# Optimization experiments

Hardware: AMD Instinct MI355X
Metric: run time of the kernel (lower is better)

## Reference

```python
import jax, jax.numpy as jnp
import numpy as np

NUM_HEADS = 12
TOP_K = 4
LN_EPS = 1e-5


def _ln(x, w, b):
    m = jnp.mean(x, -1, keepdims=True)
    v = jnp.mean((x - m) ** 2, -1, keepdims=True)
    return (x - m) * jax.lax.rsqrt(v + LN_EPS) * w + b


def _attn(x, qkv_w, qkv_b, proj_w, proj_b):
    B, N, C = x.shape
    hd = C // NUM_HEADS
    qkv = (x @ qkv_w + qkv_b).reshape(B, N, 3, NUM_HEADS, hd)
    q, k, v = jnp.moveaxis(qkv, 2, 0)  # each [B,N,H,hd]
    attn = jax.nn.softmax(jnp.einsum('bnhd,bmhd->bhnm', q * hd ** -0.5, k), axis=-1)
    out = jnp.einsum('bhnm,bmhd->bnhd', attn, v).reshape(B, N, C)
    return out @ proj_w + proj_b


def _moe(x2, gate_w, w1, b1, w2, b2):
    # x2: [tokens, D]; vmoe-style token top-k gating (eval mode, no noise)
    Tt = x2.shape[0]
    E = gate_w.shape[1]
    probs = jax.nn.softmax(x2 @ gate_w, axis=-1)            # [tokens, E]
    topv, topi = jax.lax.top_k(probs, TOP_K)                # [tokens, K]
    combine = jnp.zeros((Tt, E), x2.dtype).at[jnp.arange(Tt)[:, None], topi].set(topv)
    h = jax.nn.gelu(jnp.einsum('td,edh->teh', x2, w1) + b1[None], approximate=False)
    y = jnp.einsum('teh,ehd->ted', h, w2) + b2[None]
    return jnp.einsum('ted,te->td', y, combine)


def reference(x, ln1a_w, ln1a_b, qkv_wa, qkv_ba, proj_wa, proj_ba, ln2a_w, ln2a_b,
              fc1_w, fc1_b, fc2_w, fc2_b,
              ln1b_w, ln1b_b, qkv_wb, qkv_bb, proj_wb, proj_bb, ln2b_w, ln2b_b,
              gate_w, w1, b1, w2, b2, head_w, head_b,
              shared_masks, agg_mask):
    B, N, D = x.shape
    # dense ViT block
    x = x + _attn(_ln(x, ln1a_w, ln1a_b), qkv_wa, qkv_ba, proj_wa, proj_ba)
    h = _ln(x, ln2a_w, ln2a_b)
    x = x + (jax.nn.gelu(h @ fc1_w + fc1_b, approximate=False) @ fc2_w + fc2_b)
    # MoE ViT block
    x = x + _attn(_ln(x, ln1b_w, ln1b_b), qkv_wb, qkv_bb, proj_wb, proj_bb)
    h = _ln(x, ln2b_w, ln2b_b).reshape(B * N, D)
    x = x + _moe(h, gate_w, w1, b1, w2, b2).reshape(B, N, D)
    # per-task heads + masked multi-task aggregation (Aggregation.forward)
    task_out = jnp.einsum('bnd,tdo->tbno', x, head_w) + head_b[:, None, None, :]
    valid = (shared_masks & agg_mask[None]).astype(x.dtype)[..., None]  # [T,B,N,1]
    summed = (task_out * valid).sum(0)
    count = valid.sum(0)
    return summed / (count + 1e-6)


def setup_inputs() -> dict:
    key = jax.random.key(0)
    ks = jax.random.split(key, 32)
    B, N, D, HID, E, T = 8, 197, 768, 3072, 8, 8
    f = lambda k, shape: (jax.random.normal(k, shape, jnp.float32) * 0.02)
    return {
        'x': jax.random.normal(ks[0], (B, N, D), jnp.float32),
        'ln1a_w': jnp.ones((D,)), 'ln1a_b': jnp.zeros((D,)),
        'qkv_wa': f(ks[1], (D, 3 * D)), 'qkv_ba': jnp.zeros((3 * D,)),
        'proj_wa': f(ks[2], (D, D)), 'proj_ba': jnp.zeros((D,)),
        'ln2a_w': jnp.ones((D,)), 'ln2a_b': jnp.zeros((D,)),
        'fc1_w': f(ks[3], (D, HID)), 'fc1_b': jnp.zeros((HID,)),
        'fc2_w': f(ks[4], (HID, D)), 'fc2_b': jnp.zeros((D,)),
        'ln1b_w': jnp.ones((D,)), 'ln1b_b': jnp.zeros((D,)),
        'qkv_wb': f(ks[5], (D, 3 * D)), 'qkv_bb': jnp.zeros((3 * D,)),
        'proj_wb': f(ks[6], (D, D)), 'proj_bb': jnp.zeros((D,)),
        'ln2b_w': jnp.ones((D,)), 'ln2b_b': jnp.zeros((D,)),
        'gate_w': f(ks[7], (D, E)),
        'w1': f(ks[8], (E, D, HID)), 'b1': jnp.zeros((E, HID)),
        'w2': f(ks[9], (E, HID, D)), 'b2': jnp.zeros((E, D)),
        'head_w': f(ks[10], (T, D, D)), 'head_b': jnp.zeros((T, D)),
        'shared_masks': jax.random.bernoulli(ks[11], 0.5, (T, B, N)),
        'agg_mask': jax.random.bernoulli(ks[12], 0.5, (B, N)),
    }
```

## Files before the change

### kernel.cpp

```cpp
#include <hip/hip_runtime.h>
#include <hip/hip_bf16.h>

#define DEV static __device__ __forceinline__

typedef short bfx8 __attribute__((ext_vector_type(8)));
typedef float fx4  __attribute__((ext_vector_type(4)));

DEV float bf2f(__hip_bfloat16 h) { return __bfloat162float(h); }
DEV __hip_bfloat16 f2bf(float f) { return __float2bfloat16(f); }
DEV float uLO(unsigned u) { return __uint_as_float(u << 16); }
DEV float uHI(unsigned u) { return __uint_as_float(u & 0xffff0000u); }
DEV unsigned short f2bfu(float f) { __hip_bfloat16 h = __float2bfloat16(f); return *(unsigned short*)&h; }

DEV float wave_sum(float v) {
#pragma unroll
  for (int o = 32; o; o >>= 1) v += __shfl_xor(v, o, 64);
  return v;
}

#define GLD_LDS16(gp, lp) __builtin_amdgcn_global_load_lds( \
    (__attribute__((address_space(1))) void*)(gp),          \
    (__attribute__((address_space(3))) void*)(lp), 16, 0, 0)

__global__ __launch_bounds__(256) void transpose_k(
    const float* __restrict__ src, __hip_bfloat16* __restrict__ dst,
    int R, int C)
{
  __shared__ float tile[32][33];
  size_t off = (size_t)blockIdx.z * R * C;
  src += off; dst += off;
  int c0 = blockIdx.x * 32, r0 = blockIdx.y * 32;
#pragma unroll
  for (int i = 0; i < 32; i += 8)
    tile[threadIdx.y + i][threadIdx.x] =
        src[(size_t)(r0 + threadIdx.y + i) * C + c0 + threadIdx.x];
  __syncthreads();
#pragma unroll
  for (int i = 0; i < 32; i += 8)
    dst[(size_t)(c0 + threadIdx.y + i) * R + r0 + threadIdx.x] =
        f2bf(tile[threadIdx.x][threadIdx.y + i]);
}

enum { EPI_STORE = 0, EPI_GELU = 1, EPI_RESADD = 2, EPI_MOE = 3,
       EPI_GELU_R = 4, EPI_MOEP = 5, EPI_HEAD_R = 6 };

template <int MODE>
__global__ __launch_bounds__(256) void gemm_bt(
    const __hip_bfloat16* __restrict__ A,
    const __hip_bfloat16* __restrict__ BT,
    const float* __restrict__ bias,
    int M, int N, int K, int splitK, int taskBase,
    long long strideBz, long long strideBiasz, long long strideAz, long long strideCz,
    __hip_bfloat16* __restrict__ Cb, float* __restrict__ Cf,
    const float* __restrict__ combine, const int* __restrict__ rt)
{
  constexpr bool ROUTED = (MODE == EPI_GELU_R || MODE == EPI_MOEP || MODE == EPI_HEAD_R);
  constexpr bool GATHER = (MODE == EPI_GELU_R || MODE == EPI_HEAD_R);
  __shared__ __hip_bfloat16 sA[128 * 32];
  __shared__ __hip_bfloat16 sB[128 * 32];
  const int tid = threadIdx.x;
  const int wave = tid >> 6, lane = tid & 63;
  const int quad = lane >> 4, l16 = lane & 15;
  const int z = blockIdx.z;
  const int zt = z / splitK;
  const int kc = z - zt * splitK;
  const int task = taskBase + zt;
  const int Ksub = K / splitK;
  const int kbeg = kc * Ksub;
  const int m0 = blockIdx.y * 128, n0 = blockIdx.x * 128;

  int Meff = M;
  int rtb = 0;
  const int* ilist = nullptr;
  if (ROUTED) {
    const int base = (MODE == EPI_HEAD_R) ? 8 : 0;
    Meff = rt[base + zt];
    ilist = rt + 24 + (size_t)base * M + (size_t)zt * M;
    if (MODE == EPI_MOEP) rtb = rt[16 + zt];
    if (m0 >= Meff) return;
  }

  A += (size_t)zt * strideAz;
  if (MODE != EPI_MOEP) Cb += (size_t)zt * strideCz;
  const __hip_bfloat16* Bz = BT + (size_t)zt * strideBz;
  const float* biasz = bias + (size_t)zt * strideBiasz;
  const int wm = (wave >> 1) * 64, wn = (wave & 1) * 64;

  fx4 acc[4][4];
#pragma unroll
  for (int i = 0; i < 4; ++i)
#pragma unroll
    for (int j = 0; j < 4; ++j) acc[i][j] = (fx4){0.f, 0.f, 0.f, 0.f};

  const int c0 = tid, c1 = tid + 256;
  const int mlim = Meff - 1;
  int gm0 = m0 + (c0 >> 2); if (gm0 > mlim) gm0 = mlim;
  int gm1 = m0 + (c1 >> 2); if (gm1 > mlim) gm1 = mlim;
  const int ar0 = GATHER ? ilist[gm0] : gm0;
  const int ar1 = GATHER ? ilist[gm1] : gm1;
  const int ak0 = (c0 & 3) * 8, ak1 = (c1 & 3) * 8;
  const __hip_bfloat16* pa0 = A + (size_t)ar0 * K + kbeg + ak0;
  const __hip_bfloat16* pa1 = A + (size_t)ar1 * K + kbeg + ak1;
  const __hip_bfloat16* pb0 = Bz + (size_t)(n0 + (c0 >> 2)) * K + kbeg + ak0;
  const __hip_bfloat16* pb1 = Bz + (size_t)(n0 + (c1 >> 2)) * K + kbeg + ak1;

  for (int kk = 0; kk < Ksub; kk += 32) {
    GLD_LDS16(pa0 + kk, &sA[c0 * 8]);
    GLD_LDS16(pa1 + kk, &sA[c1 * 8]);
    GLD_LDS16(pb0 + kk, &sB[c0 * 8]);
    GLD_LDS16(pb1 + kk, &sB[c1 * 8]);
    __syncthreads();
    bfx8 af[4], bfr[4];
#pragma unroll
    for (int i = 0; i < 4; ++i)
      af[i] = *(const bfx8*)(&sA[(wm + i * 16 + l16) * 32 + quad * 8]);
#pragma unroll
    for (int j = 0; j < 4; ++j)
      bfr[j] = *(const bfx8*)(&sB[(wn + j * 16 + l16) * 32 + quad * 8]);
#pragma unroll
    for (int i = 0; i < 4; ++i)
#pragma unroll
      for (int j = 0; j < 4; ++j)
        acc[i][j] = __builtin_amdgcn_mfma_f32_16x16x32_bf16(af[i], bfr[j], acc[i][j], 0, 0, 0);
    __syncthreads();
  }

  const int mb = m0 + wm + quad * 4;
  const int nb = n0 + wn + l16;
#pragma unroll
  for (int i = 0; i < 4; ++i) {
#pragma unroll
    for (int rr = 0; rr < 4; ++rr) {
      const int m = mb + i * 16 + rr;
      if (m >= Meff) continue;
      int orow = m;
      if (MODE == EPI_HEAD_R) orow = ilist[m];
#pragma unroll
      for (int j = 0; j < 4; ++j) {
        const int n = nb + j * 16;
        float v = acc[i][j][rr];
        if (MODE == EPI_STORE) {
          Cb[(size_t)m * N + n] = f2bf(v + biasz[n]);
        } else if (MODE == EPI_GELU || MODE == EPI_GELU_R) {
          float t = v + biasz[n];
          Cb[(size_t)m * N + n] = f2bf(0.5f * t * (1.f + erff(t * 0.70710678118654752f)));
        } else if (MODE == EPI_RESADD) {
          if (kc == 0) v += biasz[n];
          atomicAdd(&Cf[(size_t)m * N + n], v);
        } else if (MODE == EPI_MOE) {
          float s = combine[m * 8 + task];
          if (s != 0.f) {
            if (kc == 0) v += biasz[n];
            atomicAdd(&Cf[(size_t)m * N + n], s * v);
          }
        } else if (MODE == EPI_MOEP) {
          if (kc == 0) v += biasz[n];
          Cf[(size_t)kc * strideCz + (size_t)(rtb + m) * N + n] = v;
        } else {
          atomicAdd(&Cf[(size_t)orow * N + n], v + biasz[n]);
        }
      }
    }
  }
}

__global__ __launch_bounds__(256) void attn_mfma_k(
    const __hip_bfloat16* __restrict__ qkvb, __hip_bfloat16* __restrict__ outb)
{
  __shared__ __align__(16) unsigned short VT[64 * 232];
  __shared__ __align__(16) unsigned short Pst[4][16 * 232];
  const int tid = threadIdx.x;
  const int chunk = blockIdx.x & 3;
  const int bh = blockIdx.x >> 2;
  const int b = bh / 12, h = bh - b * 12;
  const size_t tokBase = (size_t)b * 197;
  const __hip_bfloat16* qkvh = qkvb + tokBase * 2304 + (size_t)h * 64;

  for (int idx = tid; idx < 197 * 32; idx += 256) {
    int j = idx >> 5, dp = idx & 31;
    unsigned pv = *(const unsigned*)(qkvh + (size_t)j * 2304 + 1536 + dp * 2);
    VT[(2 * dp) * 232 + j]     = (unsigned short)(pv & 0xffffu);
    VT[(2 * dp + 1) * 232 + j] = (unsigned short)(pv >> 16);
  }
  for (int idx = tid; idx < 64 * 35; idx += 256) {
    int r = idx / 35, c = 197 + idx % 35;
    VT[r * 232 + c] = 0;
  }
  __syncthreads();

  const int wave = tid >> 6, lane = tid & 63;
  const int quad = lane >> 4, l16 = lane & 15;
  const int mt = chunk * 4 + wave;
  if (mt >= 13) return;

  {
    int r = lane >> 2, c = 208 + (lane & 3) * 4;
    *(uint2*)&Pst[wave][r * 232 + c] = (uint2){0u, 0u};
  }

  int tq = mt * 16 + l16; if (tq > 196) tq = 196;
  const bfx8 af0 = *(const bfx8*)(qkvh + (size_t)tq * 2304 + quad * 8);
  const bfx8 af1 = *(const bfx8*)(qkvh + (size_t)tq * 2304 + 32 + quad * 8);

  fx4 sv[13];
#pragma unroll
  for (int n0 = 0; n0 < 13; ++n0) {
    int tk = n0 * 16 + l16; if (tk > 196) tk = 196;
    const __hip_bfloat16* kp = qkvh + (size_t)tk * 2304 + 768;
    bfx8 bf0 = *(const bfx8*)(kp + quad * 8);
    bfx8 bf1 = *(const bfx8*)(kp + 32 + quad * 8);
    fx4 a = (fx4){0.f, 0.f, 0.f, 0.f};
    a = __builtin_amdgcn_mfma_f32_16x16x32_bf16(af0, bf0, a, 0, 0, 0);
    a = __builtin_amdgcn_mfma_f32_16x16x32_bf16(af1, bf1, a, 0, 0, 0);
    sv[n0] = a;
  }

  float inv[4];
#pragma unroll
  for (int rr = 0; rr < 4; ++rr) {
    float mx = -3.0e38f;
#pragma unroll
    for (int n0 = 0; n0 < 13; ++n0) {
      bool ok = (n0 < 12) | (l16 < 5);
      float s = ok ? sv[n0][rr] * 0.125f : -3.0e38f;
      sv[n0][rr] = s;
      mx = fmaxf(mx, s);
    }
#pragma unroll
    for (int o = 1; o < 16; o <<= 1) mx = fmaxf(mx, __shfl_xor(mx, o, 64));
    float sum = 0.f;
#pragma unroll
    for (int n0 = 0; n0 < 13; ++n0) {
      float s = sv[n0][rr];
      float e = (s > -1.0e38f) ? __expf(s - mx) : 0.f;
      sv[n0][rr] = e;
      sum += e;
    }
#pragma unroll
    for (int o = 1; o < 16; o <<= 1) sum += __shfl_xor(sum, o, 64);
    inv[rr] = 1.f / sum;
    const int row = quad * 4 + rr;
#pragma unroll
    for (int n0 = 0; n0 < 13; ++n0)
      Pst[wave][row * 232 + n0 * 16 + l16] = f2bfu(sv[n0][rr]);
  }

  fx4 pv[4];
#pragma unroll
  for (int nd = 0; nd < 4; ++nd) pv[nd] = (fx4){0.f, 0.f, 0.f, 0.f};
#pragma unroll
  for (int kk = 0; kk < 7; ++kk) {
    bfx8 paf = *(const bfx8*)&Pst[wave][l16 * 232 + kk * 32 + quad * 8];
#pragma unroll
    for (int nd = 0; nd < 4; ++nd) {
      bfx8 bfv = *(const bfx8*)&VT[(nd * 16 + l16) * 232 + kk * 32 + quad * 8];
      pv[nd] = __builtin_amdgcn_mfma_f32_16x16x32_bf16(paf, bfv, pv[nd], 0, 0, 0);
    }
  }

#pragma unroll
  for (int rr = 0; rr < 4; ++rr) {
    const int row = quad * 4 + rr;
#pragma unroll
    for (int n0 = 0; n0 < 13; ++n0) {
      float e = sv[n0][rr];
      Pst[wave][row * 232 + n0 * 16 + l16] = f2bfu(e - uLO(f2bfu(e)));
    }
  }

#pragma unroll
  for (int kk = 0; kk < 7; ++kk) {
    bfx8 paf = *(const bfx8*)&Pst[wave][l16 * 232 + kk * 32 + quad * 8];
#pragma unroll
    for (int nd = 0; nd < 4; ++nd) {
      bfx8 bfv = *(const bfx8*)&VT[(nd * 16 + l16) * 232 + kk * 32 + quad * 8];
      pv[nd] = __builtin_amdgcn_mfma_f32_16x16x32_bf16(paf, bfv, pv[nd], 0, 0, 0);
    }
  }

#pragma unroll
  for (int rr = 0; rr < 4; ++rr) {
    int m = mt * 16 + quad * 4 + rr;
    if (m > 196) continue;
    __hip_bfloat16* op = outb + (tokBase + m) * 768 + (size_t)h * 64;
#pragma unroll
    for (int nd = 0; nd < 4; ++nd)
      op[nd * 16 + l16] = f2bf(pv[nd][rr] * inv[rr]);
  }
}

__global__ __launch_bounds__(256) void ln_k(
    const float* __restrict__ xf, const float* __restrict__ w,
    const float* __restrict__ b, __hip_bfloat16* __restrict__ out, int T)
{
  int wv = threadIdx.x >> 6, lane = threadIdx.x & 63;
  int t = blockIdx.x * 4 + wv;
  if (t >= T) return;
  const float* row = xf + (size_t)t * 768;
  float v[12]; float s = 0.f;
#pragma unroll
  for (int i = 0; i < 12; ++i) { v[i] = row[lane + i * 64]; s += v[i]; }
  s = wave_sum(s);
  float mean = s * (1.f / 768.f);
  float q = 0.f;
#pragma unroll
  for (int i = 0; i < 12; ++i) { float d = v[i] - mean; q += d * d; }
  q = wave_sum(q);
  float rstd = rsqrtf(q * (1.f / 768.f) + 1e-5f);
#pragma unroll
  for (int i = 0; i < 12; ++i) {
    int d = lane + i * 64;
    out[(size_t)t * 768 + d] = f2bf((v[i] - mean) * rstd * w[d] + b[d]);
  }
}

__global__ __launch_bounds__(256) void gate_k(
    const float* __restrict__ xf, const float* __restrict__ lw,
    const float* __restrict__ lb, const float* __restrict__ gw,
    float* __restrict__ combine, int* __restrict__ rt, int* __restrict__ smap,
    __hip_bfloat16* __restrict__ lnbout, int T)
{
  int wv = threadIdx.x >> 6, lane = threadIdx.x & 63;
  int t = blockIdx.x * 4 + wv;
  if (t >= T) return;
  const float* row = xf + (size_t)t * 768;
  float v[12]; float s = 0.f;
#pragma unroll
  for (int i = 0; i < 12; ++i) { v[i] = row[lane + i * 64]; s += v[i]; }
  s = wave_sum(s);
  float mean = s * (1.f / 768.f);
  float qv = 0.f;
#pragma unroll
  for (int i = 0; i < 12; ++i) { float d = v[i] - mean; qv += d * d; }
  qv = wave_sum(qv);
  float rstd = rsqrtf(qv * (1.f / 768.f) + 1e-5f);
  float acc[8];
#pragma unroll
  for (int e = 0; e < 8; ++e) acc[e] = 0.f;
#pragma unroll
  for (int i = 0; i < 12; ++i) {
    int d = lane + i * 64;
    float xn = (v[i] - mean) * rstd * lw[d] + lb[d];
    lnbout[(size_t)t * 768 + d] = f2bf(xn);
    float4 g0 = *(const float4*)(gw + (size_t)d * 8);
    float4 g1 = *(const float4*)(gw + (size_t)d * 8 + 4);
    acc[0] += xn * g0.x; acc[1] += xn * g0.y;
    acc[2] += xn * g0.z; acc[3] += xn * g0.w;
    acc[4] += xn * g1.x; acc[5] += xn * g1.y;
    acc[6] += xn * g1.z; acc[7] += xn * g1.w;
  }
#pragma unroll
  for (int e = 0; e < 8; ++e) acc[e] = wave_sum(acc[e]);
  float mx = acc[0];
#pragma unroll
  for (int e = 1; e < 8; ++e) mx = fmaxf(mx, acc[e]);
  float p[8]; float se = 0.f;
#pragma unroll
  for (int e = 0; e < 8; ++e) { p[e] = __expf(acc[e] - mx); se += p[e]; }
  float inv = 1.f / se;
#pragma unroll
  for (int e = 0; e < 8; ++e) p[e] *= inv;
  float outv[8]; bool used[8];
#pragma unroll
  for (int e = 0; e < 8; ++e) { outv[e] = 0.f; used[e] = false; }
  for (int k = 0; k < 4; ++k) {
    int best = -1; float bv = -1.f;
#pragma unroll
    for (int e = 0; e < 8; ++e) if (!used[e] && p[e] > bv) { bv = p[e]; best = e; }
#pragma unroll
    for (int e = 0; e < 8; ++e) if (e == best) { used[e] = true; outv[e] = bv; }
  }
#pragma unroll
  for (int e = 0; e < 8; ++e) if (lane == e) combine[(size_t)t * 8 + e] = outv[e];
#pragma unroll
  for (int e = 0; e < 8; ++e)
    if (lane == e && outv[e] != 0.f) {
      int slot = atomicAdd(&rt[e], 1);
      rt[24 + e * T + slot] = t;
      smap[(size_t)t * 8 + e] = slot;
    }
}

__global__ void prefix_k(int* __restrict__ rt) {
  if (threadIdx.x == 0) {
    int s = 0;
#pragma unroll
    for (int e = 0; e < 8; ++e) { rt[16 + e] = s; s += rt[e]; }
  }
}

__global__ __launch_bounds__(256) void combine_k(
    const float* __restrict__ y, const float* __restrict__ combine,
    const int* __restrict__ rt, const int* __restrict__ smap,
    float* __restrict__ xf, int T, int CAP)
{
  int wv = threadIdx.x >> 6, lane = threadIdx.x & 63;
  int t = blockIdx.x * 4 + wv;
  if (t >= T) return;
  float acc[12];
#pragma unroll
  for (int i = 0; i < 12; ++i) acc[i] = 0.f;
  for (int e = 0; e < 8; ++e) {
    float s = combine[(size_t)t * 8 + e];
    if (s != 0.f) {
      int r = rt[16 + e] + smap[(size_t)t * 8 + e];
      const float* y0 = y + (size_t)r * 768;
      const float* y1 = y0 + (size_t)CAP * 768;
#pragma unroll
      for (int i = 0; i < 12; ++i)
        acc[i] += s * (y0[lane + i * 64] + y1[lane + i * 64]);
    }
  }
  float* xr = xf + (size_t)t * 768;
#pragma unroll
  for (int i = 0; i < 12; ++i) xr[lane + i * 64] += acc[i];
}

__global__ void mask_k(const int* __restrict__ sm, const int* __restrict__ am,
                       float* __restrict__ cnt, int* __restrict__ rt, int T)
{
  int t = blockIdx.x * 256 + threadIdx.x;
  if (t >= T) return;
  int a = am[t] != 0;
  float c = 0.f;
#pragma unroll
  for (int tt = 0; tt < 8; ++tt) {
    int vv = (sm[tt * T + t] != 0) & a;
    if (vv) {
      int slot = atomicAdd(&rt[8 + tt], 1);
      rt[24 + 8 * T + tt * T + slot] = t;
    }
    c += (float)vv;
  }
  cnt[t] = c;
}

__global__ void f2b_k(const float* __restrict__ in, __hip_bfloat16* __restrict__ out, int n) {
  int i = blockIdx.x * 256 + threadIdx.x;
  if (i < n) out[i] = f2bf(in[i]);
}
__global__ void final_k(float* __restrict__ out, const float* __restrict__ cnt, int n) {
  int i = blockIdx.x * 256 + threadIdx.x;
  if (i < n) out[i] = out[i] / (cnt[i / 768] + 1e-6f);
}

extern "C" void kernel_launch(void* const* d_in, const int* in_sizes, int n_in,
                              void* d_out, int out_size, void* d_ws, size_t ws_size,
                              hipStream_t stream)
{
  (void)in_sizes; (void)n_in; (void)out_size;
  const int Ttok = 8 * 197;
  const int D = 768, HID = 3072;
  const int CAP = 4 * Ttok;

  const float* x       = (const float*)d_in[0];
  const float* ln1a_w  = (const float*)d_in[1];
  const float* ln1a_b  = (const float*)d_in[2];
  const float* qkv_wa  = (const float*)d_in[3];
  const float* qkv_ba  = (const float*)d_in[4];
  const float* proj_wa = (const float*)d_in[5];
  const float* proj_ba = (const float*)d_in[6];
  const float* ln2a_w  = (const float*)d_in[7];
  const float* ln2a_b  = (const float*)d_in[8];
  const float* fc1_w   = (const float*)d_in[9];
  const float* fc1_b   = (const float*)d_in[10];
  const float* fc2_w   = (const float*)d_in[11];
  const float* fc2_b   = (const float*)d_in[12];
  const float* ln1b_w  = (const float*)d_in[13];
  const float* ln1b_b  = (const float*)d_in[14];
  const float* qkv_wb  = (const float*)d_in[15];
  const float* qkv_bb  = (const float*)d_in[16];
  const float* proj_wb = (const float*)d_in[17];
  const float* proj_bb = (const float*)d_in[18];
  const float* ln2b_w  = (const float*)d_in[19];
  const float* ln2b_b  = (const float*)d_in[20];
  const float* gate_w  = (const float*)d_in[21];
  const float* w1      = (const float*)d_in[22];
  const float* b1      = (const float*)d_in[23];
  const float* w2      = (const float*)d_in[24];
  const float* b2      = (const float*)d_in[25];
  const float* head_w  = (const float*)d_in[26];
  const float* head_b  = (const float*)d_in[27];
  const int* shared_masks = (const int*)d_in[28];
  const int* agg_mask     = (const int*)d_in[29];
  float* out           = (float*)d_out;

  char* wsp = (char*)d_ws;
  auto alloc = [&](size_t bytes) { char* p = wsp; wsp += (bytes + 255) & ~(size_t)255; return p; };
  float* xf             = (float*)alloc((size_t)Ttok * D * 4);
  __hip_bfloat16* lnb   = (__hip_bfloat16*)alloc((size_t)Ttok * D * 2);
  __hip_bfloat16* qkvb  = (__hip_bfloat16*)alloc((size_t)Ttok * 3 * D * 2);
  __hip_bfloat16* attnb = (__hip_bfloat16*)alloc((size_t)Ttok * D * 2);
  __hip_bfloat16* h1    = (__hip_bfloat16*)alloc((size_t)Ttok * HID * 2);
  float* combine        = (float*)alloc((size_t)Ttok * 8 * 4);
  float* cnt            = (float*)alloc((size_t)Ttok * 4);
  int* rt               = (int*)alloc((size_t)(24 + 16 * Ttok) * 4);
  int* smap             = (int*)alloc((size_t)Ttok * 8 * 4);
  __hip_bfloat16* qkvaT = (__hip_bfloat16*)alloc((size_t)D * 3 * D * 2);
  __hip_bfloat16* projaT= (__hip_bfloat16*)alloc((size_t)D * D * 2);
  __hip_bfloat16* fc1T  = (__hip_bfloat16*)alloc((size_t)D * HID * 2);
  __hip_bfloat16* fc2T  = (__hip_bfloat16*)alloc((size_t)D * HID * 2);
  __hip_bfloat16* qkvbT = (__hip_bfloat16*)alloc((size_t)D * 3 * D * 2);
  __hip_bfloat16* projbT= (__hip_bfloat16*)alloc((size_t)D * D * 2);
  __hip_bfloat16* headT = (__hip_bfloat16*)alloc((size_t)8 * D * D * 2);
  __hip_bfloat16* wT    = (__hip_bfloat16*)alloc((size_t)D * HID * 2);

  const size_t used = (size_t)(wsp - (char*)d_ws);
  const size_t extraNeed = 2 * ((size_t)8 * D * HID * 2 + 255)
                         + ((size_t)8 * Ttok * HID * 2 + 255)
                         + (2 * (size_t)CAP * D * 4 + 255);
  const bool batched = (ws_size >= used + extraNeed);
  __hip_bfloat16* w1T8 = nullptr; __hip_bfloat16* w2T8 = nullptr; __hip_bfloat16* h1_8 = nullptr;
  float* yb = nullptr;
  if (batched) {
    w1T8 = (__hip_bfloat16*)alloc((size_t)8 * D * HID * 2);
    w2T8 = (__hip_bfloat16*)alloc((size_t)8 * D * HID * 2);
    h1_8 = (__hip_bfloat16*)alloc((size_t)8 * Ttok * HID * 2);
    yb   = (float*)alloc(2 * (size_t)CAP * D * 4);
  }

  dim3 tb(32, 8);
  transpose_k<<<dim3(3*D/32, D/32, 1), tb, 0, stream>>>(qkv_wa, qkvaT, D, 3*D);
  transpose_k<<<dim3(D/32, D/32, 1),   tb, 0, stream>>>(proj_wa, projaT, D, D);
  transpose_k<<<dim3(HID/32, D/32, 1), tb, 0, stream>>>(fc1_w, fc1T, D, HID);
  transpose_k<<<dim3(D/32, HID/32, 1), tb, 0, stream>>>(fc2_w, fc2T, HID, D);
  transpose_k<<<dim3(3*D/32, D/32, 1), tb, 0, stream>>>(qkv_wb, qkvbT, D, 3*D);
  transpose_k<<<dim3(D/32, D/32, 1),   tb, 0, stream>>>(proj_wb, projbT, D, D);
  transpose_k<<<dim3(D/32, D/32, 8),   tb, 0, stream>>>(head_w, headT, D, D);
  if (batched) {
    transpose_k<<<dim3(HID/32, D/32, 8), tb, 0, stream>>>(w1, w1T8, D, HID);
    transpose_k<<<dim3(D/32, HID/32, 8), tb, 0, stream>>>(w2, w2T8, HID, D);
  }

  const int nTok = Ttok * D;
  hipMemcpyAsync(xf, x, (size_t)nTok * 4, hipMemcpyDeviceToDevice, stream);
  hipMemsetAsync(rt, 0, 64, stream);
  mask_k<<<(Ttok + 255)/256, 256, 0, stream>>>(shared_masks, agg_mask, cnt, rt, Ttok);
  hipMemsetAsync(out, 0, (size_t)nTok * 4, stream);

  const int lnGrid = (Ttok + 3) / 4;
  dim3 g_qkv(3*D/128, 13, 1);
  dim3 g_proj(D/128, 13, 4);
  dim3 g_fc1(HID/128, 13, 1);
  dim3 g_fc2(D/128, 13, 4);
  dim3 g_head(D/128, 13, 8);
  const int attnGrid = 96 * 4;

  ln_k<<<lnGrid, 256, 0, stream>>>(xf, ln1a_w, ln1a_b, lnb, Ttok);
  gemm_bt<EPI_STORE><<<g_qkv, 256, 0, stream>>>(lnb, qkvaT, qkv_ba, Ttok, 3*D, D, 1, 0, 0, 0, 0, 0, qkvb, nullptr, nullptr, nullptr);
  attn_mfma_k<<<attnGrid, 256, 0, stream>>>(qkvb, attnb);
  gemm_bt<EPI_RESADD><<<g_proj, 256, 0, stream>>>(attnb, projaT, proj_ba, Ttok, D, D, 4, 0, 0, 0, 0, 0, nullptr, xf, nullptr, nullptr);
  ln_k<<<lnGrid, 256, 0, stream>>>(xf, ln2a_w, ln2a_b, lnb, Ttok);
  gemm_bt<EPI_GELU><<<g_fc1, 256, 0, stream>>>(lnb, fc1T, fc1_b, Ttok, HID, D, 1, 0, 0, 0, 0, 0, h1, nullptr, nullptr, nullptr);
  gemm_bt<EPI_RESADD><<<g_fc2, 256, 0, stream>>>(h1, fc2T, fc2_b, Ttok, D, HID, 4, 0, 0, 0, 0, 0, nullptr, xf, nullptr, nullptr);

  ln_k<<<lnGrid, 256, 0, stream>>>(xf, ln1b_w, ln1b_b, lnb, Ttok);
  gemm_bt<EPI_STORE><<<g_qkv, 256, 0, stream>>>(lnb, qkvbT, qkv_bb, Ttok, 3*D, D, 1, 0, 0, 0, 0, 0, qkvb, nullptr, nullptr, nullptr);
  attn_mfma_k<<<attnGrid, 256, 0, stream>>>(qkvb, attnb);
  gemm_bt<EPI_RESADD><<<g_proj, 256, 0, stream>>>(attnb, projbT, proj_bb, Ttok, D, D, 4, 0, 0, 0, 0, 0, nullptr, xf, nullptr, nullptr);
  gate_k<<<lnGrid, 256, 0, stream>>>(xf, ln2b_w, ln2b_b, gate_w, combine, rt, smap, lnb, Ttok);
  prefix_k<<<1, 64, 0, stream>>>(rt);
  if (batched) {
    gemm_bt<EPI_GELU_R><<<dim3(HID/128, 13, 8), 256, 0, stream>>>(
        lnb, w1T8, b1, Ttok, HID, D, 1, 0,
        (long long)D*HID, HID, 0, (long long)Ttok*HID, h1_8, nullptr, nullptr, rt);
    gemm_bt<EPI_MOEP><<<dim3(D/128, 13, 16), 256, 0, stream>>>(
        h1_8, w2T8, b2, Ttok, D, HID, 2, 0,
        (long long)HID*D, D, (long long)Ttok*HID, (long long)CAP*D, nullptr, yb, nullptr, rt);
    combine_k<<<lnGrid, 256, 0, stream>>>(yb, combine, rt, smap, xf, Ttok, CAP);
  } else {
    for (int e = 0; e < 8; ++e) {
      transpose_k<<<dim3(HID/32, D/32, 1), tb, 0, stream>>>(w1 + (size_t)e*D*HID, wT, D, HID);
      gemm_bt<EPI_GELU><<<g_fc1, 256, 0, stream>>>(lnb, wT, b1 + (size_t)e*HID, Ttok, HID, D, 1, 0, 0, 0, 0, 0, h1, nullptr, nullptr, nullptr);
      transpose_k<<<dim3(D/32, HID/32, 1), tb, 0, stream>>>(w2 + (size_t)e*HID*D, wT, HID, D);
      gemm_bt<EPI_MOE><<<g_fc2, 256, 0, stream>>>(h1, wT, b2 + (size_t)e*D, Ttok, D, HID, 4, e, 0, 0, 0, 0, nullptr, xf, combine, nullptr);
    }
  }

  f2b_k<<<(nTok + 255)/256, 256, 0, stream>>>(xf, lnb, nTok);
  gemm_bt<EPI_HEAD_R><<<g_head, 256, 0, stream>>>(lnb, headT, head_b, Ttok, D, D, 1, 0, (long long)D*D, D, 0, 0, nullptr, out, nullptr, rt);
  final_k<<<(nTok + 255)/256, 256, 0, stream>>>(out, cnt, nTok);
}
```

Measured before the change: 870.2 us.

## Double-buffer GEMM LDS tiles, batch weight transposes, fuse bf16 cast into combine

The GEMM k-loop now double-buffers its A and B LDS tiles, so global-to-LDS loads for the next k-step are issued while MFMAs run on the current one, and one barrier per iteration is removed. The nine weight transpose launches are merged into one kernel driven by a descriptor table. The combine kernel also writes the bf16 copy of the residual, which removes a separate f2b pass in the batched path. The cost is doubled GEMM LDS use (32KB per block), which may lower occupancy.

Result: faster. 834.3 us (-4.1%).

```diff
diff --git a/kernel.cpp b/kernel.cpp
--- a/kernel.cpp
+++ b/kernel.cpp
@@ -9,7 +9,6 @@
 DEV float bf2f(__hip_bfloat16 h) { return __bfloat162float(h); }
 DEV __hip_bfloat16 f2bf(float f) { return __float2bfloat16(f); }
 DEV float uLO(unsigned u) { return __uint_as_float(u << 16); }
-DEV float uHI(unsigned u) { return __uint_as_float(u & 0xffff0000u); }
 DEV unsigned short f2bfu(float f) { __hip_bfloat16 h = __float2bfloat16(f); return *(unsigned short*)&h; }
 
 DEV float wave_sum(float v) {
@@ -21,6 +20,36 @@
 #define GLD_LDS16(gp, lp) __builtin_amdgcn_global_load_lds( \
     (__attribute__((address_space(1))) void*)(gp),          \
     (__attribute__((address_space(3))) void*)(lp), 16, 0, 0)
+
+struct TDesc { const float* src; __hip_bfloat16* dst; int R, C, nz, tilesPerZ, tileOff; };
+struct TPack { TDesc d[9]; int n; };
+
+__global__ __launch_bounds__(256) void transpose_all_k(TPack p) {
+  __shared__ float tile[32][33];
+  const int bid = blockIdx.x;
+  int di = 0;
+#pragma unroll
+  for (int i = 1; i < 9; ++i)
+    if (i < p.n && bid >= p.d[i].tileOff) di = i;
+  const TDesc d = p.d[di];
+  int local = bid - d.tileOff;
+  int z = local / d.tilesPerZ;
+  int rem = local - z * d.tilesPerZ;
+  int ctiles = d.C >> 5;
+  int bx = rem % ctiles, by = rem / ctiles;
+  const float* src = d.src + (size_t)z * d.R * d.C;
+  __hip_bfloat16* dst = d.dst + (size_t)z * d.R * d.C;
+  int c0 = bx * 32, r0 = by * 32;
+#pragma unroll
+  for (int i = 0; i < 32; i += 8)
+    tile[threadIdx.y + i][threadIdx.x] =
+        src[(size_t)(r0 + threadIdx.y + i) * d.C + c0 + threadIdx.x];
+  __syncthreads();
+#pragma unroll
+  for (int i = 0; i < 32; i += 8)
+    dst[(size_t)(c0 + threadIdx.y + i) * d.R + r0 + threadIdx.x] =
+        f2bf(tile[threadIdx.x][threadIdx.y + i]);
+}
 
 __global__ __launch_bounds__(256) void transpose_k(
     const float* __restrict__ src, __hip_bfloat16* __restrict__ dst,
@@ -56,8 +85,8 @@
 {
   constexpr bool ROUTED = (MODE == EPI_GELU_R || MODE == EPI_MOEP || MODE == EPI_HEAD_R);
   constexpr bool GATHER = (MODE == EPI_GELU_R || MODE == EPI_HEAD_R);
-  __shared__ __hip_bfloat16 sA[128 * 32];
-  __shared__ __hip_bfloat16 sB[128 * 32];
+  __shared__ __hip_bfloat16 sA[2][128 * 32];
+  __shared__ __hip_bfloat16 sB[2][128 * 32];
   const int tid = threadIdx.x;
   const int wave = tid >> 6, lane = tid & 63;
   const int quad = lane >> 4, l16 = lane & 15;
@@ -104,25 +133,35 @@
   const __hip_bfloat16* pb0 = Bz + (size_t)(n0 + (c0 >> 2)) * K + kbeg + ak0;
   const __hip_bfloat16* pb1 = Bz + (size_t)(n0 + (c1 >> 2)) * K + kbeg + ak1;
 
+  GLD_LDS16(pa0, &sA[0][c0 * 8]);
+  GLD_LDS16(pa1, &sA[0][c1 * 8]);
+  GLD_LDS16(pb0, &sB[0][c0 * 8]);
+  GLD_LDS16(pb1, &sB[0][c1 * 8]);
+  __syncthreads();
+
+  int cur = 0;
   for (int kk = 0; kk < Ksub; kk += 32) {
-    GLD_LDS16(pa0 + kk, &sA[c0 * 8]);
-    GLD_LDS16(pa1 + kk, &sA[c1 * 8]);
-    GLD_LDS16(pb0 + kk, &sB[c0 * 8]);
-    GLD_LDS16(pb1 + kk, &sB[c1 * 8]);
-    __syncthreads();
+    const int nxt = kk + 32;
+    if (nxt < Ksub) {
+      GLD_LDS16(pa0 + nxt, &sA[cur ^ 1][c0 * 8]);
+      GLD_LDS16(pa1 + nxt, &sA[cur ^ 1][c1 * 8]);
+      GLD_LDS16(pb0 + nxt, &sB[cur ^ 1][c0 * 8]);
+      GLD_LDS16(pb1 + nxt, &sB[cur ^ 1][c1 * 8]);
+    }
     bfx8 af[4], bfr[4];
 #pragma unroll
     for (int i = 0; i < 4; ++i)
-      af[i] = *(const bfx8*)(&sA[(wm + i * 16 + l16) * 32 + quad * 8]);
+      af[i] = *(const bfx8*)(&sA[cur][(wm + i * 16 + l16) * 32 + quad * 8]);
 #pragma unroll
     for (int j = 0; j < 4; ++j)
-      bfr[j] = *(const bfx8*)(&sB[(wn + j * 16 + l16) * 32 + quad * 8]);
+      bfr[j] = *(const bfx8*)(&sB[cur][(wn + j * 16 + l16) * 32 + quad * 8]);
 #pragma unroll
     for (int i = 0; i < 4; ++i)
 #pragma unroll
       for (int j = 0; j < 4; ++j)
         acc[i][j] = __builtin_amdgcn_mfma_f32_16x16x32_bf16(af[i], bfr[j], acc[i][j], 0, 0, 0);
     __syncthreads();
+    cur ^= 1;
   }
 
   const int mb = m0 + wm + quad * 4;
@@ -392,7 +431,7 @@
 __global__ __launch_bounds__(256) void combine_k(
     const float* __restrict__ y, const float* __restrict__ combine,
     const int* __restrict__ rt, const int* __restrict__ smap,
-    float* __restrict__ xf, int T, int CAP)
+    float* __restrict__ xf, __hip_bfloat16* __restrict__ lnbout, int T, int CAP)
 {
   int wv = threadIdx.x >> 6, lane = threadIdx.x & 63;
   int t = blockIdx.x * 4 + wv;
@@ -413,7 +452,11 @@
   }
   float* xr = xf + (size_t)t * 768;
 #pragma unroll
-  for (int i = 0; i < 12; ++i) xr[lane + i * 64] += acc[i];
+  for (int i = 0; i < 12; ++i) {
+    float nv = xr[lane + i * 64] + acc[i];
+    xr[lane + i * 64] = nv;
+    lnbout[(size_t)t * 768 + lane + i * 64] = f2bf(nv);
+  }
 }
 
 __global__ void mask_k(const int* __restrict__ sm, const int* __restrict__ am,
@@ -520,16 +563,32 @@
   }
 
   dim3 tb(32, 8);
-  transpose_k<<<dim3(3*D/32, D/32, 1), tb, 0, stream>>>(qkv_wa, qkvaT, D, 3*D);
-  transpose_k<<<dim3(D/32, D/32, 1),   tb, 0, stream>>>(proj_wa, projaT, D, D);
-  transpose_k<<<dim3(HID/32, D/32, 1), tb, 0, stream>>>(fc1_w, fc1T, D, HID);
-  transpose_k<<<dim3(D/32, HID/32, 1), tb, 0, stream>>>(fc2_w, fc2T, HID, D);
-  transpose_k<<<dim3(3*D/32, D/32, 1), tb, 0, stream>>>(qkv_wb, qkvbT, D, 3*D);
-  transpose_k<<<dim3(D/32, D/32, 1),   tb, 0, stream>>>(proj_wb, projbT, D, D);
-  transpose_k<<<dim3(D/32, D/32, 8),   tb, 0, stream>>>(head_w, headT, D, D);
   if (batched) {
-    transpose_k<<<dim3(HID/32, D/32, 8), tb, 0, stream>>>(w1, w1T8, D, HID);
-    transpose_k<<<dim3(D/32, HID/32, 8), tb, 0, stream>>>(w2, w2T8, HID, D);
+    TPack p; int off = 0;
+    auto addT = [&](int i, const float* s, __hip_bfloat16* dd, int R, int C, int nz) {
+      int tpz = (R / 32) * (C / 32);
+      p.d[i] = TDesc{s, dd, R, C, nz, tpz, off};
+      off += tpz * nz;
+    };
+    addT(0, qkv_wa, qkvaT, D, 3 * D, 1);
+    addT(1, proj_wa, projaT, D, D, 1);
+    addT(2, fc1_w, fc1T, D, HID, 1);
+    addT(3, fc2_w, fc2T, HID, D, 1);
+    addT(4, qkv_wb, qkvbT, D, 3 * D, 1);
+    addT(5, proj_wb, projbT, D, D, 1);
+    addT(6, head_w, headT, D, D, 8);
+    addT(7, w1, w1T8, D, HID, 8);
+    addT(8, w2, w2T8, HID, D, 8);
+    p.n = 9;
+    transpose_all_k<<<off, tb, 0, stream>>>(p);
+  } else {
+    transpose_k<<<dim3(3*D/32, D/32, 1), tb, 0, stream>>>(qkv_wa, qkvaT, D, 3*D);
+    transpose_k<<<dim3(D/32, D/32, 1),   tb, 0, stream>>>(proj_wa, projaT, D, D);
+    transpose_k<<<dim3(HID/32, D/32, 1), tb, 0, stream>>>(fc1_w, fc1T, D, HID);
+    transpose_k<<<dim3(D/32, HID/32, 1), tb, 0, stream>>>(fc2_w, fc2T, HID, D);
+    transpose_k<<<dim3(3*D/32, D/32, 1), tb, 0, stream>>>(qkv_wb, qkvbT, D, 3*D);
+    transpose_k<<<dim3(D/32, D/32, 1),   tb, 0, stream>>>(proj_wb, projbT, D, D);
+    transpose_k<<<dim3(D/32, D/32, 8),   tb, 0, stream>>>(head_w, headT, D, D);
   }
 
   const int nTok = Ttok * D;
@@ -567,7 +626,7 @@
     gemm_bt<EPI_MOEP><<<dim3(D/128, 13, 16), 256, 0, stream>>>(
         h1_8, w2T8, b2, Ttok, D, HID, 2, 0,
         (long long)HID*D, D, (long long)Ttok*HID, (long long)CAP*D, nullptr, yb, nullptr, rt);
-    combine_k<<<lnGrid, 256, 0, stream>>>(yb, combine, rt, smap, xf, Ttok, CAP);
+    combine_k<<<lnGrid, 256, 0, stream>>>(yb, combine, rt, smap, xf, lnb, Ttok, CAP);
   } else {
     for (int e = 0; e < 8; ++e) {
       transpose_k<<<dim3(HID/32, D/32, 1), tb, 0, stream>>>(w1 + (size_t)e*D*HID, wT, D, HID);
@@ -575,9 +634,9 @@
       transpose_k<<<dim3(D/32, HID/32, 1), tb, 0, stream>>>(w2 + (size_t)e*HID*D, wT, HID, D);
       gemm_bt<EPI_MOE><<<g_fc2, 256, 0, stream>>>(h1, wT, b2 + (size_t)e*D, Ttok, D, HID, 4, e, 0, 0, 0, 0, nullptr, xf, combine, nullptr);
     }
-  }
-
-  f2b_k<<<(nTok + 255)/256, 256, 0, stream>>>(xf, lnb, nTok);
+    f2b_k<<<(nTok + 255)/256, 256, 0, stream>>>(xf, lnb, nTok);
+  }
+
   gemm_bt<EPI_HEAD_R><<<g_head, 256, 0, stream>>>(lnb, headT, head_b, Ttok, D, D, 1, 0, (long long)D*D, D, 0, 0, nullptr, out, nullptr, rt);
   final_k<<<(nTok + 255)/256, 256, 0, stream>>>(out, cnt, nTok);
 }
```
